# Kernel tuning notes

Measured on AMD Instinct MI355X. Metric: run time of the kernel, lower is better.

Reference implementation:

```python
import jax, jax.numpy as jnp
import numpy as np

B = 2
ROW, COL = 63, 84          # resolution
ROW_, COL_ = 32, 42        # resolution_
N = ROW * COL              # 5292 kv tokens
N_ = ROW_ * COL_           # 1344 q tokens
IN_DIM, OUT_DIM = 256, 512
KEY_DIM, NUM_HEADS, ATTN_RATIO, STRIDE = 16, 8, 2, 2
D = ATTN_RATIO * KEY_DIM   # 32 (value dim per head)
DH = D * NUM_HEADS         # 256
NH_KD = KEY_DIM * NUM_HEADS  # 128
H_KV = DH + NH_KD          # 384
SCALE = KEY_DIM ** -0.5
EPS = 1e-5


def _build_bias_idxs():
    # replicates the itertools.product double loop, vectorized; ids ordered by
    # first occurrence in row-major scan (same as dict insertion order).
    r_ = np.arange(ROW_); c_ = np.arange(COL_)
    r = np.arange(ROW); c = np.arange(COL)
    off_r = np.abs(r_[:, None] * STRIDE - r[None, :])      # (32, 63)
    off_c = np.abs(c_[:, None] * STRIDE - c[None, :])      # (42, 84)
    keys = (off_r[:, None, :, None] * 1000 + off_c[None, :, None, :]).reshape(-1)
    _, first_idx, inv = np.unique(keys, return_index=True, return_inverse=True)
    order = np.argsort(first_idx)
    rank = np.empty_like(order); rank[order] = np.arange(len(order))
    idxs = rank[inv].reshape(N_, N).astype(np.int32)
    return idxs, len(order)


def setup_inputs() -> dict:
    key = jax.random.key(0)
    ks = jax.random.split(key, 12)
    idxs_np, n_off = _build_bias_idxs()
    inp = {
        "x": jax.random.normal(ks[0], (B, N, IN_DIM), jnp.float32),
        "kv_w": jax.random.normal(ks[1], (H_KV, IN_DIM), jnp.float32) * (IN_DIM ** -0.5),
        "kv_g": jnp.ones((H_KV,), jnp.float32),
        "kv_b": jnp.zeros((H_KV,), jnp.float32),
        "q_w": jax.random.normal(ks[2], (NH_KD, IN_DIM), jnp.float32) * (IN_DIM ** -0.5),
        "q_g": jnp.ones((NH_KD,), jnp.float32),
        "q_b": jnp.zeros((NH_KD,), jnp.float32),
        "proj_w": jax.random.normal(ks[3], (OUT_DIM, DH), jnp.float32) * (DH ** -0.5),
        "proj_g": jnp.ones((OUT_DIM,), jnp.float32),
        "proj_b": jnp.zeros((OUT_DIM,), jnp.float32),
        "bias_table": jax.random.normal(ks[4], (NUM_HEADS, n_off), jnp.float32) * 0.02,
        "bias_idxs": jnp.asarray(idxs_np),
    }
    return inp


def _linear_bn(x, w, g, b):
    # Linear (no bias) followed by BatchNorm1d in training mode (batch stats
    # over flattened (B*N) dim, biased variance).
    y = jnp.einsum("bnc,oc->bno", x, w)
    flat = y.reshape(-1, y.shape[-1])
    mu = flat.mean(0)
    var = flat.var(0)
    return (y - mu) * (g / jnp.sqrt(var + EPS)) + b


def _hardswish(x):
    return x * jnp.clip(x + 3.0, 0.0, 6.0) / 6.0


def reference(x, kv_w, kv_g, kv_b, q_w, q_g, q_b, proj_w, proj_g, proj_b,
              bias_table, bias_idxs):
    Bx = x.shape[0]
    # kv projection -> split k (KEY_DIM) and v (D) per head
    kv = _linear_bn(x, kv_w, kv_g, kv_b).reshape(Bx, N, NUM_HEADS, KEY_DIM + D)
    k = kv[..., :KEY_DIM].transpose(0, 2, 1, 3)   # (B, H, N, key_dim)
    v = kv[..., KEY_DIM:].transpose(0, 2, 1, 3)   # (B, H, N, d)
    # q: spatial subsample then projection
    xs = x.reshape(Bx, ROW, COL, IN_DIM)[:, ::STRIDE, ::STRIDE].reshape(Bx, N_, IN_DIM)
    q = _linear_bn(xs, q_w, q_g, q_b).reshape(Bx, N_, NUM_HEADS, KEY_DIM).transpose(0, 2, 1, 3)
    # gathered relative position bias: (H, N_, N)
    ab = bias_table[:, bias_idxs]
    attn = jnp.einsum("bhqd,bhkd->bhqk", q, k) * SCALE + ab[None]
    attn = jax.nn.softmax(attn, axis=-1)
    out = jnp.einsum("bhqk,bhkd->bhqd", attn, v)       # (B, H, N_, d)
    out = out.transpose(0, 2, 1, 3).reshape(Bx, N_, DH)
    out = _linear_bn(_hardswish(out), proj_w, proj_g, proj_b)
    return out
```

## Files before the change

kernel.cpp:

```cpp
#include <hip/hip_runtime.h>
#include <hip/hip_bf16.h>
#include <math.h>

#define N_K 5292
#define N_KP 5376
#define N_Q 1344
#define NH_KD 128
#define NROWS 21504
#define LOG2E 1.4426950408889634f
#define MSTAT 16.0f

typedef float f32x4 __attribute__((ext_vector_type(4)));
typedef short short8 __attribute__((ext_vector_type(8)));

__device__ __forceinline__ float fexp2(float x) {
#if __has_builtin(__builtin_amdgcn_exp2f)
    return __builtin_amdgcn_exp2f(x);
#else
    return exp2f(x);
#endif
}

__device__ __forceinline__ unsigned pk_bf16(float a, float b) {
    union { __hip_bfloat162 h; unsigned u; } c;
    c.h = __float22bfloat162_rn(make_float2(a, b));
    return c.u;
}
__device__ __forceinline__ unsigned short f2bf(float a) {
    return (unsigned short)pk_bf16(a, 0.f);
}

__global__ __launch_bounds__(256) void prep_bf16(
    const float* __restrict__ X, const float* __restrict__ kv_w,
    const float* __restrict__ q_w,
    unsigned short* __restrict__ Xb, float* __restrict__ sums)
{
    int i = blockIdx.x * 256 + threadIdx.x;
    if (i >= 710144) {
        int j = i - 710144;
        float4 z = make_float4(0.f, 0.f, 0.f, 0.f);
        *(float4*)(sums + (size_t)j * 8)     = z;
        *(float4*)(sums + (size_t)j * 8 + 4) = z;
        return;
    }
    const float* src;
    long off;
    if (i < 677376)       { src = X;      off = i; }
    else if (i < 701952)  { src = kv_w;   off = i - 677376; }
    else                  { src = q_w;    off = i - 701952; }
    float4 v = *(const float4*)(src + off * 4);
    *(uint2*)(Xb + (size_t)i * 4) = make_uint2(pk_bf16(v.x, v.y), pk_bf16(v.z, v.w));
}

__device__ __forceinline__ void gemm_body128(
    const unsigned short* __restrict__ A, const unsigned short* __restrict__ W,
    long asrc, long bsrc,
    unsigned short (*As)[40], unsigned short (*Bs)[40], f32x4 acc[4][4])
{
    const int t = threadIdx.x;
    const int w = t >> 6, lane = t & 63, g = lane >> 4, ln = lane & 15;
    const int wr = w >> 1, wc = w & 1;
    const int srow = t >> 1;
    const int sc16 = (t & 1) * 16;

    uint4 a0 = make_uint4(0,0,0,0), a1 = make_uint4(0,0,0,0);
    if (asrc >= 0) {
        a0 = *(const uint4*)(A + asrc * 256 + sc16);
        a1 = *(const uint4*)(A + asrc * 256 + sc16 + 8);
    }
    uint4 b0 = *(const uint4*)(W + bsrc * 256 + sc16);
    uint4 b1 = *(const uint4*)(W + bsrc * 256 + sc16 + 8);

    #pragma unroll
    for (int k0 = 0; k0 < 256; k0 += 32) {
        __syncthreads();
        *(uint4*)&As[srow][sc16]     = a0;
        *(uint4*)&As[srow][sc16 + 8] = a1;
        *(uint4*)&Bs[srow][sc16]     = b0;
        *(uint4*)&Bs[srow][sc16 + 8] = b1;
        __syncthreads();

        if (k0 < 224) {
            if (asrc >= 0) {
                a0 = *(const uint4*)(A + asrc * 256 + k0 + 32 + sc16);
                a1 = *(const uint4*)(A + asrc * 256 + k0 + 32 + sc16 + 8);
            }
            b0 = *(const uint4*)(W + bsrc * 256 + k0 + 32 + sc16);
            b1 = *(const uint4*)(W + bsrc * 256 + k0 + 32 + sc16 + 8);
        }

        short8 af[4], bf[4];
        #pragma unroll
        for (int mi = 0; mi < 4; ++mi)
            af[mi] = *(const short8*)&As[wr * 64 + mi * 16 + ln][g * 8];
        #pragma unroll
        for (int ni = 0; ni < 4; ++ni)
            bf[ni] = *(const short8*)&Bs[wc * 64 + ni * 16 + ln][g * 8];
        #pragma unroll
        for (int mi = 0; mi < 4; ++mi)
            #pragma unroll
            for (int ni = 0; ni < 4; ++ni)
                acc[mi][ni] = __builtin_amdgcn_mfma_f32_16x16x32_bf16(
                    af[mi], bf[ni], acc[mi][ni], 0, 0, 0);
    }
}

__device__ __forceinline__ void gemm_stats128(f32x4 acc[4][4], float* __restrict__ sums,
                                              int n0, int Ncols, float* scratch)
{
    const int t = threadIdx.x;
    const int w = t >> 6, lane = t & 63, g = lane >> 4, ln = lane & 15;
    float sA[4], qA[4];
    #pragma unroll
    for (int ni = 0; ni < 4; ++ni) {
        float s = 0.f, q = 0.f;
        #pragma unroll
        for (int mi = 0; mi < 4; ++mi)
            #pragma unroll
            for (int r = 0; r < 4; ++r) {
                float v = acc[mi][ni][r];
                s += v; q = fmaf(v, v, q);
            }
        s += __shfl_xor(s, 16); s += __shfl_xor(s, 32);
        q += __shfl_xor(q, 16); q += __shfl_xor(q, 32);
        sA[ni] = s; qA[ni] = q;
    }
    __syncthreads();
    float* st_s = scratch;
    float* st_q = scratch + 256;
    if (g == 0) {
        #pragma unroll
        for (int ni = 0; ni < 4; ++ni) {
            st_s[(w * 4 + ni) * 16 + ln] = sA[ni];
            st_q[(w * 4 + ni) * 16 + ln] = qA[ni];
        }
    }
    __syncthreads();
    if (t < 128) {
        int wc = t >> 6, nl = t & 63;
        float a  = st_s[wc * 64 + nl] + st_s[(wc + 2) * 64 + nl];
        float b2 = st_q[wc * 64 + nl] + st_q[(wc + 2) * 64 + nl];
        atomicAdd(&sums[n0 + t], a);
        atomicAdd(&sums[Ncols + n0 + t], b2);
    }
}

__global__ __launch_bounds__(256) void gemm_qkv(
    const unsigned short* __restrict__ Xb, const unsigned short* __restrict__ kvWb,
    const unsigned short* __restrict__ qWb,
    const float* __restrict__ bias_table, const int* __restrict__ bias_idxs, int n_off,
    unsigned short* __restrict__ Kp, unsigned short* __restrict__ Vpt,
    float* __restrict__ bt_r,
    float* __restrict__ q_y, float* __restrict__ sums_kv, float* __restrict__ sums_q)
{
    __shared__ unsigned short As[128][40], Bs[128][40];
    const int t = threadIdx.x;
    const int w = t >> 6, lane = t & 63, g = lane >> 4, ln = lane & 15;
    const int wr = w >> 1, wc = w & 1;
    const int srow = t >> 1;
    int id = blockIdx.x;

    if (id >= 270) {
        id -= 270;
        if (id < 168) {
            int i = id * 256 + t;
            int row = i / 84, j = i - row * 84;
            int slot;
            if (j < 20) {
                int kap = 44 + j;
                slot = 5248 + (((kap & 15) << 2) | (kap >> 4));
            } else {
                slot = 5312 + (j - 20);
            }
            Vpt[(size_t)row * N_KP + slot] = 0;
        } else {
            int i = (id - 168) * 256 + t;
            if (i < 8 * N_K) {
                int h = i / N_K, j = i - h * N_K;
                bt_r[i] = bias_table[h * n_off + bias_idxs[j]] * LOG2E;
            }
        }
        return;
    }

    f32x4 acc[4][4];
    #pragma unroll
    for (int mi = 0; mi < 4; ++mi)
        #pragma unroll
        for (int ni = 0; ni < 4; ++ni) acc[mi][ni] = (f32x4){0.f, 0.f, 0.f, 0.f};

    if (id < 249) {
        const int my = id / 3, ny = id % 3;
        const int m0 = my * 128, n0 = ny * 128;
        int mrow = m0 + srow;
        long asrc = (mrow < 10584) ? mrow : -1;
        gemm_body128(Xb, kvWb, asrc, n0 + srow, As, Bs, acc);

        #pragma unroll
        for (int ni = 0; ni < 4; ++ni) {
            int c = n0 + wc * 64 + ni * 16 + ln;
            int hh = c / 48, cc = c - 48 * hh;
            #pragma unroll
            for (int mi = 0; mi < 4; ++mi) {
                #pragma unroll
                for (int reg = 0; reg < 4; ++reg) {
                    int mr = m0 + wr * 64 + mi * 16 + g * 4 + reg;
                    if (mr < 10584) {
                        int bb = mr >= N_K;
                        int key = mr - bb * N_K;
                        unsigned short v16 = f2bf(acc[mi][ni][reg]);
                        if (cc < 16) {
                            Kp[((size_t)(bb * 8 + hh) * N_K + key) * 16 + cc] = v16;
                        } else {
                            int kap = key & 63;
                            int keyp = (key & ~63) | (((kap & 15) << 2) | (kap >> 4));
                            Vpt[((size_t)(bb * 8 + hh) * 32 + cc - 16) * N_KP + keyp] = v16;
                        }
                    }
                }
            }
        }
        gemm_stats128(acc, sums_kv, n0, 384, (float*)&As[0][0]);
    } else {
        const int my = id - 249;
        const int m0 = my * 128;
        int mrow = m0 + srow;
        int bb = mrow / N_Q;
        int i = mrow - bb * N_Q;
        long asrc = (long)(bb * N_K + (i / 42) * 168 + (i % 42) * 2);
        gemm_body128(Xb, qWb, asrc, srow, As, Bs, acc);

        #pragma unroll
        for (int ni = 0; ni < 4; ++ni) {
            int c = wc * 64 + ni * 16 + ln;
            #pragma unroll
            for (int mi = 0; mi < 4; ++mi)
                #pragma unroll
                for (int reg = 0; reg < 4; ++reg) {
                    int mr = m0 + wr * 64 + mi * 16 + g * 4 + reg;
                    q_y[(size_t)mr * 128 + c] = acc[mi][ni][reg];
                }
        }
        gemm_stats128(acc, sums_q, 0, 128, (float*)&As[0][0]);
    }
}

__global__ __launch_bounds__(256) void gemm_proj(
    const unsigned short* __restrict__ Ap, const unsigned short* __restrict__ Wp,
    float* __restrict__ Y, float* __restrict__ sums)
{
    __shared__ unsigned short As[128][40], Bs[128][40];
    const int t = threadIdx.x;
    const int w = t >> 6, lane = t & 63, g = lane >> 4, ln = lane & 15;
    const int wr = w >> 1, wc = w & 1;
    const int srow = t >> 1;
    const int my = blockIdx.x / 4, ny = blockIdx.x % 4;
    const int m0 = my * 128, n0 = ny * 128;

    f32x4 acc[4][4];
    #pragma unroll
    for (int mi = 0; mi < 4; ++mi)
        #pragma unroll
        for (int ni = 0; ni < 4; ++ni) acc[mi][ni] = (f32x4){0.f, 0.f, 0.f, 0.f};
    gemm_body128(Ap, Wp, m0 + srow, n0 + srow, As, Bs, acc);

    #pragma unroll
    for (int ni = 0; ni < 4; ++ni) {
        int c = n0 + wc * 64 + ni * 16 + ln;
        #pragma unroll
        for (int mi = 0; mi < 4; ++mi)
            #pragma unroll
            for (int reg = 0; reg < 4; ++reg) {
                int mr = m0 + wr * 64 + mi * 16 + g * 4 + reg;
                Y[(size_t)mr * 512 + c] = acc[mi][ni][reg];
            }
    }
    gemm_stats128(acc, sums, n0, 512, (float*)&As[0][0]);
}

__global__ __launch_bounds__(256, 4) void attn_mfma(
    const unsigned short* __restrict__ Kp, const unsigned short* __restrict__ Vpt,
    const float* __restrict__ q_y, const float* __restrict__ sums_q,
    const float* __restrict__ q_g, const float* __restrict__ q_b,
    const float* __restrict__ sums_kv, const float* __restrict__ kv_g,
    const float* __restrict__ bt_r,
    float* __restrict__ pl, float* __restrict__ pacc)
{
    const int id = blockIdx.x;
    const int h = id & 7;
    const int z = (id >> 3) & 7;
    const int qt = id >> 6;
    const int b = z >> 2, ks = z & 3;
    const int t = threadIdx.x;
    const int w = t >> 6, lane = t & 63, g = lane >> 4, ln = lane & 15;

    __shared__ float btm_s[21 * 166];
    __shared__ unsigned short K_s[2][64][24];
    __shared__ unsigned short Vt_s[2][32][72];
    __shared__ unsigned short P_s[4][16][72];

    const int q0 = qt * 64;
    const int kstart = ks * 1344;
    const int kend = (kstart + 1344 < N_K) ? kstart + 1344 : N_K;
    const int ntiles = (kend - kstart + 63) >> 6;
    const bool tail = (ks == 3);

    const int kr0 = kstart / 84;
    const int kr1 = (kend - 1) / 84;
    const int rq2min = (q0 / 42) * 2;
    const int rq2max = ((q0 + 63) / 42) * 2;
    const int dmin_r = rq2min - kr1;
    const int rows = (rq2max - kr0) - dmin_r + 1;
    const int nb = rows * 166;
    const unsigned mxb = (unsigned)((nb - 1) * 4);
    {
        const float* src = bt_r + h * N_K;
        for (int j = t; j < nb; j += 256) {
            int rr = j / 166, ii = j - rr * 166;
            int dr = dmin_r + rr; dr = dr < 0 ? -dr : dr;
            int dc = ii - 83; dc = dc < 0 ? -dc : dc;
            btm_s[j] = src[dr * 84 + dc];
        }
    }

    short8 qfrag = (short8)0;
    if (lane < 32) {
        const float invq = 1.f / 2688.f, invk = 1.f / 10584.f;
        const float post = 0.25f * LOG2E;
        const int c0 = h * 16 + g * 8;
        const int ck = h * 48 + g * 8;
        const float* qp = q_y + (size_t)(b * N_Q + q0 + w * 16 + ln) * NH_KD + c0;
        float vv[8];
        #pragma unroll
        for (int j = 0; j < 8; ++j) {
            float mu  = sums_q[c0 + j] * invq;
            float var = fmaf(-mu, mu, sums_q[128 + c0 + j] * invq);
            float s   = q_g[c0 + j] * rsqrtf(var + 1e-5f) * post;
            float vq  = fmaf(qp[j], s, fmaf(-mu, s, q_b[c0 + j] * post));
            float muk = sums_kv[ck + j] * invk;
            float vrk = fmaf(-muk, muk, sums_kv[384 + ck + j] * invk);
            float sk  = kv_g[ck + j] * rsqrtf(vrk + 1e-5f);
            vv[j] = vq * sk;
        }
        union { short8 s; unsigned u[4]; } qf;
        qf.u[0] = pk_bf16(vv[0], vv[1]); qf.u[1] = pk_bf16(vv[2], vv[3]);
        qf.u[2] = pk_bf16(vv[4], vv[5]); qf.u[3] = pk_bf16(vv[6], vv[7]);
        qfrag = qf.s;
    }

    union { short8 s; unsigned u[4]; } onef;
    #pragma unroll
    for (int j = 0; j < 4; ++j) onef.u[j] = 0x3F803F80u;
    const short8 ones = onef.s;

    int baseb[4];
    #pragma unroll
    for (int reg = 0; reg < 4; ++reg) {
        int qg = q0 + w * 16 + g * 4 + reg;
        int rq2 = (qg / 42) * 2;
        int cq2 = (qg % 42) * 2;
        baseb[reg] = ((rq2 - dmin_r) * 166 + cq2 + 83) * 4;
    }
    int offb[4], kcc[4];
    #pragma unroll
    for (int st = 0; st < 4; ++st) {
        int kg = kstart + st * 16 + ln;
        int okr = kg / 84;
        kcc[st] = kg - okr * 84;
        offb[st] = -(okr * 166 + kcc[st]) * 4;
    }

    const unsigned* kp_base = (const unsigned*)Kp + (size_t)(b * 8 + h) * N_K * 8;
    const int skey = t >> 2, schunk = t & 3;
    const int vrow = t >> 3, vc8 = (t & 7) * 8;
    const unsigned short* vptr = Vpt + (size_t)(b * 8 + h) * 32 * N_KP
                                     + (size_t)vrow * N_KP + kstart + vc8;

    uint2 kreg; uint4 vreg;
    {
        int kg = kstart + skey; if (kg > N_K - 1) kg = N_K - 1;
        kreg = *(const uint2*)(kp_base + (size_t)kg * 8 + schunk * 2);
        vreg = *(const uint4*)vptr;
    }
    *(uint2*)&K_s[0][skey][schunk * 4] = kreg;
    *(uint4*)&Vt_s[0][vrow][vc8] = vreg;
    __syncthreads();

    f32x4 acc0 = {0.f, 0.f, 0.f, 0.f}, acc1 = {0.f, 0.f, 0.f, 0.f};
    f32x4 accL = {0.f, 0.f, 0.f, 0.f};
    const f32x4 minit = {-MSTAT, -MSTAT, -MSTAT, -MSTAT};
    int p = 0;

    for (int it = 0; it < ntiles; ++it) {
        const int k0 = kstart + it * 64;
        const bool notlast = (it + 1 < ntiles);
        if (notlast) {
            int kg = k0 + 64 + skey; if (kg > N_K - 1) kg = N_K - 1;
            kreg = *(const uint2*)(kp_base + (size_t)kg * 8 + schunk * 2);
            vreg = *(const uint4*)(vptr + 64);
        }

        f32x4 sf[4];
        #pragma unroll
        for (int st = 0; st < 4; ++st) {
            short8 bf = (short8)0;
            if (lane < 32) bf = *(const short8*)&K_s[p][st * 16 + ln][g * 8];
            sf[st] = __builtin_amdgcn_mfma_f32_16x16x32_bf16(qfrag, bf, minit, 0, 0, 0);
        }

        float pv[4][4];
        const bool clampit = tail && (it == ntiles - 1);
        if (!clampit) {
            #pragma unroll
            for (int st = 0; st < 4; ++st) {
                #pragma unroll
                for (int reg = 0; reg < 4; ++reg) {
                    unsigned ub = (unsigned)(baseb[reg] + offb[st]);
                    float bias = *(const float*)((const char*)btm_s + ub);
                    pv[st][reg] = fexp2(sf[st][reg] + bias);
                }
            }
        } else {
            #pragma unroll
            for (int st = 0; st < 4; ++st) {
                bool bad = (k0 + st * 16 + ln) >= N_K;
                #pragma unroll
                for (int reg = 0; reg < 4; ++reg) {
                    unsigned ub = (unsigned)(baseb[reg] + offb[st]);
                    ub = ub > mxb ? mxb : ub;
                    float bias = *(const float*)((const char*)btm_s + ub);
                    pv[st][reg] = bad ? 0.f : fexp2(sf[st][reg] + bias);
                }
            }
        }

        #pragma unroll
        for (int reg = 0; reg < 4; ++reg) {
            uint2 pw = make_uint2(pk_bf16(pv[0][reg], pv[1][reg]),
                                  pk_bf16(pv[2][reg], pv[3][reg]));
            *(uint2*)&P_s[w][g * 4 + reg][4 * ln] = pw;
        }
        __asm__ __volatile__("" ::: "memory");

        #pragma unroll
        for (int kt = 0; kt < 2; ++kt) {
            short8 af = *(const short8*)&P_s[w][ln][g * 8 + kt * 32];
            short8 b0 = *(const short8*)&Vt_s[p][ln][g * 8 + kt * 32];
            short8 b1 = *(const short8*)&Vt_s[p][ln + 16][g * 8 + kt * 32];
            acc0 = __builtin_amdgcn_mfma_f32_16x16x32_bf16(af, b0, acc0, 0, 0, 0);
            acc1 = __builtin_amdgcn_mfma_f32_16x16x32_bf16(af, b1, acc1, 0, 0, 0);
            accL = __builtin_amdgcn_mfma_f32_16x16x32_bf16(af, ones, accL, 0, 0, 0);
        }

        if (notlast) {
            int q2 = p ^ 1;
            *(uint2*)&K_s[q2][skey][schunk * 4] = kreg;
            *(uint4*)&Vt_s[q2][vrow][vc8] = vreg;
            __syncthreads();
            p = q2;
            vptr += 64;
        }

        #pragma unroll
        for (int st = 0; st < 4; ++st) {
            kcc[st] += 64;
            if (kcc[st] >= 84) { kcc[st] -= 84; offb[st] -= 584; }
            else offb[st] -= 256;
        }
    }

    const int rbase = (b * 8 + h) * N_Q + q0 + w * 16;
    #pragma unroll
    for (int reg = 0; reg < 4; ++reg) {
        int prow = ks * NROWS + rbase + g * 4 + reg;
        pacc[(size_t)prow * 32 + ln]      = acc0[reg];
        pacc[(size_t)prow * 32 + 16 + ln] = acc1[reg];
        if (ln == 0) pl[prow] = accL[reg];
    }
}

__global__ __launch_bounds__(256) void combine_kernel(const float* __restrict__ pl,
                                                      const float* __restrict__ pacc,
                                                      const float* __restrict__ sums_kv,
                                                      const float* __restrict__ kv_g,
                                                      const float* __restrict__ kv_b,
                                                      unsigned short* __restrict__ attn_o,
                                                      const float* __restrict__ proj_w,
                                                      unsigned short* __restrict__ projWb)
{
    if (blockIdx.x >= 672) {
        int i = (blockIdx.x - 672) * 256 + threadIdx.x;
        float4 v = *(const float4*)(proj_w + (size_t)i * 4);
        *(uint2*)(projWb + (size_t)i * 4) = make_uint2(pk_bf16(v.x, v.y), pk_bf16(v.z, v.w));
        return;
    }
    int idx = blockIdx.x * 256 + threadIdx.x;
    int r = idx >> 3, e4 = (idx & 7) * 4;
    float L = (pl[r] + pl[NROWS + r]) + (pl[2 * NROWS + r] + pl[3 * NROWS + r]);
    float invL = 1.f / L;
    size_t o = (size_t)r * 32 + e4;
    float4 v0 = *(const float4*)(pacc + o);
    float4 v1 = *(const float4*)(pacc + (size_t)NROWS * 32 + o);
    float4 v2 = *(const float4*)(pacc + (size_t)2 * NROWS * 32 + o);
    float4 v3 = *(const float4*)(pacc + (size_t)3 * NROWS * 32 + o);
    int q = r % N_Q;
    int bh = r / N_Q;
    int hh = bh & 7, b = bh >> 3;
    const int ch = hh * 48 + 16 + e4;
    const float invk = 1.f / 10584.f;
    float hs[4];
    #pragma unroll
    for (int u = 0; u < 4; ++u) {
        float v = (u == 0 ? v0.x + v1.x + v2.x + v3.x :
                   u == 1 ? v0.y + v1.y + v2.y + v3.y :
                   u == 2 ? v0.z + v1.z + v2.z + v3.z :
                            v0.w + v1.w + v2.w + v3.w);
        float mu  = sums_kv[ch + u] * invk;
        float var = fmaf(-mu, mu, sums_kv[384 + ch + u] * invk);
        float s   = kv_g[ch + u] * rsqrtf(var + 1e-5f);
        float tt  = fmaf(-mu, s, kv_b[ch + u]);
        v = fmaf(s, v * invL, tt);
        hs[u] = v * fminf(fmaxf(v + 3.f, 0.f), 6.f) * (1.f / 6.f);
    }
    *(uint2*)(attn_o + (size_t)(b * N_Q + q) * 256 + hh * 32 + e4) =
        make_uint2(pk_bf16(hs[0], hs[1]), pk_bf16(hs[2], hs[3]));
}

__global__ __launch_bounds__(256) void norm_apply(
    const float* __restrict__ Y, const float* __restrict__ sums,
    const float* __restrict__ g, const float* __restrict__ bb,
    float* __restrict__ out, int rows, int cols, float inv_rows)
{
    __shared__ float sc_s[64], sh_s[64];
    const int t = threadIdx.x;
    const int c0 = blockIdx.x * 64;
    if (t < 64) {
        int c = c0 + t;
        float mu  = sums[c] * inv_rows;
        float var = fmaf(-mu, mu, sums[cols + c] * inv_rows);
        float s   = g[c] * rsqrtf(var + 1e-5f);
        sc_s[t] = s;
        sh_s[t] = fmaf(-mu, s, bb[c]);
    }
    __syncthreads();
    const int c4 = (t & 15) * 4;
    float4 scv = *(const float4*)&sc_s[c4];
    float4 shv = *(const float4*)&sh_s[c4];
    for (int r = blockIdx.y * 16 + (t >> 4); r < rows; r += gridDim.y * 16) {
        size_t off = (size_t)r * cols + c0 + c4;
        float4 v = *(const float4*)(Y + off);
        v.x = fmaf(v.x, scv.x, shv.x);
        v.y = fmaf(v.y, scv.y, shv.y);
        v.z = fmaf(v.z, scv.z, shv.z);
        v.w = fmaf(v.w, scv.w, shv.w);
        *(float4*)(out + off) = v;
    }
}

extern "C" void kernel_launch(void* const* d_in, const int* in_sizes, int n_in,
                              void* d_out, int out_size, void* d_ws, size_t ws_size,
                              hipStream_t stream) {
    (void)n_in; (void)out_size; (void)ws_size;
    const float* x      = (const float*)d_in[0];
    const float* kv_w   = (const float*)d_in[1];
    const float* kv_g   = (const float*)d_in[2];
    const float* kv_b   = (const float*)d_in[3];
    const float* q_w    = (const float*)d_in[4];
    const float* q_g    = (const float*)d_in[5];
    const float* q_b    = (const float*)d_in[6];
    const float* proj_w = (const float*)d_in[7];
    const float* proj_g = (const float*)d_in[8];
    const float* proj_b = (const float*)d_in[9];
    const float* bias_table = (const float*)d_in[10];
    const int*   bias_idxs  = (const int*)d_in[11];
    const int    n_off = in_sizes[10] / 8;
    float* out = (float*)d_out;

    float* ws = (float*)d_ws;
    float* q_y  = ws;
    float* pacc = q_y + 2688 * 128;
    float* proj_y = pacc;
    float* pl = pacc + 4 * NROWS * 32;
    unsigned short* attn_o = (unsigned short*)(pl + 4 * NROWS);
    unsigned short* Kp  = attn_o + 2688 * 256;
    unsigned short* Vpt = Kp + 2 * 8 * N_K * 16;
    float* sums_kv = (float*)(Vpt + 2 * 8 * 32 * N_KP);
    float* sums_q  = sums_kv + 768;
    float* sums_p  = sums_q + 256;
    float* bt_r    = sums_p + 1024;

    unsigned short* Xb     = (unsigned short*)pacc;
    unsigned short* kvWb   = Xb + 10584 * 256;
    unsigned short* qWb    = kvWb + 384 * 256;
    unsigned short* projWb = (unsigned short*)q_y;

    prep_bf16<<<2775, 256, 0, stream>>>(x, kv_w, q_w, Xb, sums_kv);
    gemm_qkv<<<270 + 168 + 166, 256, 0, stream>>>(Xb, kvWb, qWb, bias_table, bias_idxs,
                                                  n_off, Kp, Vpt, bt_r,
                                                  q_y, sums_kv, sums_q);
    attn_mfma<<<1344, 256, 0, stream>>>(Kp, Vpt, q_y, sums_q, q_g, q_b,
                                        sums_kv, kv_g, bt_r, pl, pacc);
    combine_kernel<<<672 + 128, 256, 0, stream>>>(pl, pacc, sums_kv, kv_g, kv_b, attn_o,
                                                  proj_w, projWb);
    gemm_proj<<<84, 256, 0, stream>>>(attn_o, projWb, proj_y, sums_p);
    norm_apply<<<dim3(8, 84), 256, 0, stream>>>(proj_y, sums_p, proj_g, proj_b, out,
                                                2688, 512, 1.f / 2688.f);
}
```

Before: 189.4 us.

## Software-pipeline QK^T one tile ahead and prefetch K two tiles ahead

Restructures the attention main loop so the QK^T MFMAs for the next key tile are issued before the bias-add, exp and PV work of the current tile. K is now loaded two tiles ahead and V one tile ahead, with clamped addresses, and double-buffered shared-memory indices are derived from the iteration parity. The aim is to overlap matrix-core latency with the exp and bias-gather ALU work and to hide global-load latency. In exchange it holds an extra score fragment in registers, which may lower occupancy. It also issues a barrier and redundant clamped loads on every iteration, including the last.

```diff
diff --git a/kernel.cpp b/kernel.cpp
--- a/kernel.cpp
+++ b/kernel.cpp
@@ -371,41 +371,51 @@
     }
 
     const unsigned* kp_base = (const unsigned*)Kp + (size_t)(b * 8 + h) * N_K * 8;
+    const unsigned short* vp_base = Vpt + (size_t)(b * 8 + h) * 32 * N_KP;
     const int skey = t >> 2, schunk = t & 3;
     const int vrow = t >> 3, vc8 = (t & 7) * 8;
-    const unsigned short* vptr = Vpt + (size_t)(b * 8 + h) * 32 * N_KP
-                                     + (size_t)vrow * N_KP + kstart + vc8;
-
-    uint2 kreg; uint4 vreg;
+
+    #define KLOAD(tile) ({ int kg_ = kstart + (tile) * 64 + skey; \
+                           if (kg_ > N_K - 1) kg_ = N_K - 1; \
+                           *(const uint2*)(kp_base + (size_t)kg_ * 8 + schunk * 2); })
+    #define VLOAD(tile) ({ int off_ = kstart + (tile) * 64; \
+                           if (off_ > N_KP - 64) off_ = N_KP - 64; \
+                           *(const uint4*)(vp_base + (size_t)vrow * N_KP + off_ + vc8); })
+
     {
-        int kg = kstart + skey; if (kg > N_K - 1) kg = N_K - 1;
-        kreg = *(const uint2*)(kp_base + (size_t)kg * 8 + schunk * 2);
-        vreg = *(const uint4*)vptr;
-    }
-    *(uint2*)&K_s[0][skey][schunk * 4] = kreg;
-    *(uint4*)&Vt_s[0][vrow][vc8] = vreg;
+        uint2 k0r = KLOAD(0);
+        uint2 k1r = KLOAD(1);
+        uint4 v0r = VLOAD(0);
+        *(uint2*)&K_s[0][skey][schunk * 4] = k0r;
+        *(uint2*)&K_s[1][skey][schunk * 4] = k1r;
+        *(uint4*)&Vt_s[0][vrow][vc8] = v0r;
+    }
     __syncthreads();
+
+    const f32x4 minit = {-MSTAT, -MSTAT, -MSTAT, -MSTAT};
+    f32x4 sf[4];
+    #pragma unroll
+    for (int st = 0; st < 4; ++st) {
+        short8 bf = (short8)0;
+        if (lane < 32) bf = *(const short8*)&K_s[0][st * 16 + ln][g * 8];
+        sf[st] = __builtin_amdgcn_mfma_f32_16x16x32_bf16(qfrag, bf, minit, 0, 0, 0);
+    }
+    uint2 kreg = KLOAD(2);
+    uint4 vreg = VLOAD(1);
 
     f32x4 acc0 = {0.f, 0.f, 0.f, 0.f}, acc1 = {0.f, 0.f, 0.f, 0.f};
     f32x4 accL = {0.f, 0.f, 0.f, 0.f};
-    const f32x4 minit = {-MSTAT, -MSTAT, -MSTAT, -MSTAT};
-    int p = 0;
 
     for (int it = 0; it < ntiles; ++it) {
-        const int k0 = kstart + it * 64;
-        const bool notlast = (it + 1 < ntiles);
-        if (notlast) {
-            int kg = k0 + 64 + skey; if (kg > N_K - 1) kg = N_K - 1;
-            kreg = *(const uint2*)(kp_base + (size_t)kg * 8 + schunk * 2);
-            vreg = *(const uint4*)(vptr + 64);
-        }
-
-        f32x4 sf[4];
-        #pragma unroll
-        for (int st = 0; st < 4; ++st) {
-            short8 bf = (short8)0;
-            if (lane < 32) bf = *(const short8*)&K_s[p][st * 16 + ln][g * 8];
-            sf[st] = __builtin_amdgcn_mfma_f32_16x16x32_bf16(qfrag, bf, minit, 0, 0, 0);
+        f32x4 sfn[4];
+        if (it + 1 < ntiles) {
+            const int pb = (it + 1) & 1;
+            #pragma unroll
+            for (int st = 0; st < 4; ++st) {
+                short8 bf = (short8)0;
+                if (lane < 32) bf = *(const short8*)&K_s[pb][st * 16 + ln][g * 8];
+                sfn[st] = __builtin_amdgcn_mfma_f32_16x16x32_bf16(qfrag, bf, minit, 0, 0, 0);
+            }
         }
 
         float pv[4][4];
@@ -421,9 +431,10 @@
                 }
             }
         } else {
+            const int k0g = kstart + it * 64;
             #pragma unroll
             for (int st = 0; st < 4; ++st) {
-                bool bad = (k0 + st * 16 + ln) >= N_K;
+                bool bad = (k0g + st * 16 + ln) >= N_K;
                 #pragma unroll
                 for (int reg = 0; reg < 4; ++reg) {
                     unsigned ub = (unsigned)(baseb[reg] + offb[st]);
@@ -442,32 +453,35 @@
         }
         __asm__ __volatile__("" ::: "memory");
 
+        const int pv_ = it & 1;
         #pragma unroll
         for (int kt = 0; kt < 2; ++kt) {
             short8 af = *(const short8*)&P_s[w][ln][g * 8 + kt * 32];
-            short8 b0 = *(const short8*)&Vt_s[p][ln][g * 8 + kt * 32];
-            short8 b1 = *(const short8*)&Vt_s[p][ln + 16][g * 8 + kt * 32];
+            short8 b0 = *(const short8*)&Vt_s[pv_][ln][g * 8 + kt * 32];
+            short8 b1 = *(const short8*)&Vt_s[pv_][ln + 16][g * 8 + kt * 32];
             acc0 = __builtin_amdgcn_mfma_f32_16x16x32_bf16(af, b0, acc0, 0, 0, 0);
             acc1 = __builtin_amdgcn_mfma_f32_16x16x32_bf16(af, b1, acc1, 0, 0, 0);
             accL = __builtin_amdgcn_mfma_f32_16x16x32_bf16(af, ones, accL, 0, 0, 0);
         }
 
-        if (notlast) {
-            int q2 = p ^ 1;
-            *(uint2*)&K_s[q2][skey][schunk * 4] = kreg;
-            *(uint4*)&Vt_s[q2][vrow][vc8] = vreg;
-            __syncthreads();
-            p = q2;
-            vptr += 64;
-        }
+        *(uint2*)&K_s[it & 1][skey][schunk * 4] = kreg;
+        *(uint4*)&Vt_s[(it + 1) & 1][vrow][vc8] = vreg;
+
+        kreg = KLOAD(it + 3);
+        vreg = VLOAD(it + 2);
+
+        __syncthreads();
 
         #pragma unroll
         for (int st = 0; st < 4; ++st) {
+            sf[st] = sfn[st];
             kcc[st] += 64;
             if (kcc[st] >= 84) { kcc[st] -= 84; offb[st] -= 584; }
             else offb[st] -= 256;
         }
     }
+    #undef KLOAD
+    #undef VLOAD
 
     const int rbase = (b * 8 + h) * N_Q + q0 + w * 16;
     #pragma unroll
```

Measured after the change: 191.6 us. About the same (+1.1%).
